# Optimization experiments

Hardware: AMD Instinct MI355X
Metric: run time of the kernel (lower is better)

The kernel has to match this reference:

```python
import jax, jax.numpy as jnp
import numpy as np

QMIN, QMAX = 0, 255        # 8-bit asymmetric activation quant bounds
GROUP_SIZE = 128

def setup_inputs() -> dict:
    key = jax.random.key(0)
    k1, k2, k3, k4, k5 = jax.random.split(key, 5)
    x = jax.random.normal(k1, (1, 2048, 4096), dtype=jnp.float32)
    qweight = jax.random.randint(k2, (4096, 32, 128), 0, 16, dtype=jnp.int32)  # uint4 codes
    w_scales = jax.random.uniform(k3, (4096, 32), dtype=jnp.float32, minval=0.001, maxval=0.02)
    w_zero_points = jax.random.randint(k4, (4096, 32), 0, 16, dtype=jnp.int32)
    bias = jax.random.normal(k5, (4096,), dtype=jnp.float32)
    return {"x": x, "qweight": qweight, "w_scales": w_scales,
            "w_zero_points": w_zero_points, "bias": bias}

def reference(x, qweight, w_scales, w_zero_points, bias):
    xf = x.astype(jnp.float32)
    # per-token (last-dim) asymmetric dynamic activation quantization
    xmin = jnp.min(xf, axis=-1, keepdims=True)
    xmax = jnp.max(xf, axis=-1, keepdims=True)
    x_scale = jnp.clip((xmax - xmin) / (QMAX - QMIN), 1e-5, None)
    x_zp = jnp.clip(jnp.round(-xmin / x_scale), QMIN, QMAX)
    q = jnp.clip(jnp.round(xf / x_scale) + x_zp, QMIN, QMAX)
    centered_x = (q - x_zp).reshape(*x.shape[:-1], -1, GROUP_SIZE)  # [B,S,G,C]
    # grouped weight dequant (zero-point centered)
    centered_w = qweight.astype(jnp.float32) - w_zero_points.astype(jnp.float32)[..., None]  # [O,G,C]
    acc = jnp.einsum('bsgc,ogc->bsog', centered_x, centered_w)  # [B,S,O,G]
    out = (acc * w_scales[None, None]).sum(axis=-1)  # apply per-group weight scales
    out = out * x_scale  # per-token activation scale
    out = out + bias
    return out
```

## Files before the change

kernel.cpp:

```cpp
#include <hip/hip_runtime.h>
#include <stdint.h>

#define M_DIM 2048
#define N_DIM 4096
#define K_DIM 4096
#define NGROUP 32
#define GSIZE 128

#define RQ_UP   (127.0f / 15.0f)
#define RQ_DOWN (15.0f / 127.0f)

#define BM 128
#define BN 128
#define KSLICE 64
#define NSLICE (K_DIM / KSLICE)
#define ASLOT (BM * KSLICE)
#define BSLOT (BN * KSLICE)

typedef __attribute__((ext_vector_type(4))) int int32x4_t;

static __device__ __forceinline__ void gl2lds16(const void* g, void* l) {
    auto gp = (const __attribute__((address_space(1))) unsigned int*)(uintptr_t)g;
    auto lp = (__attribute__((address_space(3))) unsigned int*)(uintptr_t)l;
    __builtin_amdgcn_global_load_lds(gp, lp, 16, 0, 0);
}

#define WAITVM_(N) asm volatile("s_waitcnt vmcnt(" #N ")" ::: "memory")
#define WAITVM(N) WAITVM_(N)
#define WAITLGKM_(N) asm volatile("s_waitcnt lgkmcnt(" #N ")" ::: "memory")
#define WAITLGKM(N) WAITLGKM_(N)
#define BARRIER() asm volatile("s_barrier" ::: "memory")

#define QUANT_BLOCKS M_DIM
#define DEQ_BLOCKS ((N_DIM * K_DIM) / 8 / 256)

__global__ __launch_bounds__(256) void prep_kernel(
        const float* __restrict__ x,
        const int* __restrict__ qw,
        const float* __restrict__ wsc,
        const int* __restrict__ wzp,
        char* __restrict__ A8,
        char* __restrict__ Bt8,
        float* __restrict__ xscale,
        float* __restrict__ xzpc,
        int* __restrict__ Sw)
{
    const int t = threadIdx.x;
    if (blockIdx.x < QUANT_BLOCKS) {
        const int s = blockIdx.x;
        const float* xrow = x + (size_t)s * K_DIM;

        float xv[16];
        float vmin = 1e38f, vmax = -1e38f;
#pragma unroll
        for (int p = 0; p < 4; ++p) {
            float4 v = *((const float4*)(xrow + p * 1024) + t);
            xv[p*4+0] = v.x; xv[p*4+1] = v.y; xv[p*4+2] = v.z; xv[p*4+3] = v.w;
            vmin = fminf(vmin, fminf(fminf(v.x, v.y), fminf(v.z, v.w)));
            vmax = fmaxf(vmax, fmaxf(fmaxf(v.x, v.y), fmaxf(v.z, v.w)));
        }
#pragma unroll
        for (int off = 32; off > 0; off >>= 1) {
            vmin = fminf(vmin, __shfl_xor(vmin, off));
            vmax = fmaxf(vmax, __shfl_xor(vmax, off));
        }
        __shared__ float smin[4], smax[4];
        const int wave = t >> 6;
        if ((t & 63) == 0) { smin[wave] = vmin; smax[wave] = vmax; }
        __syncthreads();
        vmin = fminf(fminf(smin[0], smin[1]), fminf(smin[2], smin[3]));
        vmax = fmaxf(fmaxf(smax[0], smax[1]), fmaxf(smax[2], smax[3]));

        float sc = (vmax - vmin) / 255.0f;
        sc = fmaxf(sc, 1e-5f);
        float zp = rintf(-vmin / sc);
        zp = fminf(fmaxf(zp, 0.0f), 255.0f);

#pragma unroll
        for (int p = 0; p < 4; ++p) {
            int b[4];
#pragma unroll
            for (int e = 0; e < 4; ++e) {
                float q = fminf(fmaxf(rintf(xv[p*4+e] / sc) + zp, 0.0f), 255.0f);
                b[e] = (int)q - 128;
            }
            unsigned pack = (b[0] & 0xff) | ((b[1] & 0xff) << 8) |
                            ((b[2] & 0xff) << 16) | ((b[3] & 0xff) << 24);
            *(unsigned*)(A8 + (size_t)s * K_DIM + p * 1024 + t * 4) = pack;
        }
        if (t == 0) { xscale[s] = sc; xzpc[s] = 128.0f - zp; }
    } else {
        const size_t base = ((size_t)(blockIdx.x - QUANT_BLOCKS) * 256 + t) * 8;
        const int n = (int)(base >> 12);
        const int g = (int)((base >> 7) & 31);
        const int zp = wzp[n * NGROUP + g];

        const int cl = t & 15;
        float2 wp = *(const float2*)(wsc + (size_t)n * NGROUP + cl * 2);
        float smx = fmaxf(wp.x, wp.y);
#pragma unroll
        for (int off = 1; off < 16; off <<= 1)
            smx = fmaxf(smx, __shfl_xor(smx, off));
        const float factor = wsc[n * NGROUP + g] * (RQ_UP / smx);

        int4 c0 = *(const int4*)(qw + base);
        int4 c1 = *(const int4*)(qw + base + 4);
        int w[8];
        w[0] = (int)rintf((float)(c0.x - zp) * factor);
        w[1] = (int)rintf((float)(c0.y - zp) * factor);
        w[2] = (int)rintf((float)(c0.z - zp) * factor);
        w[3] = (int)rintf((float)(c0.w - zp) * factor);
        w[4] = (int)rintf((float)(c1.x - zp) * factor);
        w[5] = (int)rintf((float)(c1.y - zp) * factor);
        w[6] = (int)rintf((float)(c1.z - zp) * factor);
        w[7] = (int)rintf((float)(c1.w - zp) * factor);
        uint2 pk;
        pk.x = (w[0] & 0xff) | ((w[1] & 0xff) << 8) | ((w[2] & 0xff) << 16) | ((w[3] & 0xff) << 24);
        pk.y = (w[4] & 0xff) | ((w[5] & 0xff) << 8) | ((w[6] & 0xff) << 16) | ((w[7] & 0xff) << 24);
        *(uint2*)(Bt8 + base) = pk;

        int s8 = w[0] + w[1] + w[2] + w[3] + w[4] + w[5] + w[6] + w[7];
#pragma unroll
        for (int off = 1; off < 16; off <<= 1) s8 += __shfl_xor(s8, off);
        if ((t & 15) == 0)
            Sw[n * NGROUP + g] = s8;
    }
}

__global__ __launch_bounds__(256, 2) void gemm_kernel(
        const char* __restrict__ A8,
        const char* __restrict__ Bt8,
        const float* __restrict__ xscale,
        const float* __restrict__ xzpc,
        const float* __restrict__ wsc,
        const int* __restrict__ Sw,
        const float* __restrict__ bias,
        float* __restrict__ out)
{
    __shared__ __align__(16) char As[4][ASLOT];
    __shared__ __align__(16) char Bs[4][BSLOT];
    __shared__ float fws_s[BN], wsf_s[BN];

    const int tid  = threadIdx.x;
    const int bn   = blockIdx.x;
    const int bm   = blockIdx.y;
    const int wave = tid >> 6;
    const int lane = tid & 63;
    const int wr   = wave >> 1;
    const int wcl  = wave & 1;
    const int lrow  = lane & 15;
    const int lquad = lane >> 4;

    if (tid < BN) {
        const int n = bn * BN + tid;
        const int4* s4 = (const int4*)(Sw + (size_t)n * NGROUP);
        int acc = 0;
#pragma unroll
        for (int p = 0; p < 8; ++p) { int4 v = s4[p]; acc += v.x + v.y + v.z + v.w; }
        const float4* w4 = (const float4*)(wsc + (size_t)n * NGROUP);
        float s = 0.f;
#pragma unroll
        for (int p = 0; p < 8; ++p) {
            float4 w = w4[p];
            s = fmaxf(s, fmaxf(fmaxf(w.x, w.y), fmaxf(w.z, w.w)));
        }
        const float fw = s * RQ_DOWN;
        fws_s[tid] = fw;
        wsf_s[tid] = fw * (float)acc;
    }
    asm volatile("s_waitcnt vmcnt(0) lgkmcnt(0)" ::: "memory");

    const char* Ab = A8  + (size_t)(bm * BM) * K_DIM;
    const char* Bb = Bt8 + (size_t)(bn * BN) * K_DIM;
    const int lsub = lane >> 2;
    const int csrc = (lane & 3) ^ ((lane >> 3) & 3);
    const char* gA0 = Ab + (size_t)((wave * 16     ) + lsub) * K_DIM + csrc * 16;
    const char* gA1 = Ab + (size_t)((wave * 16 + 64) + lsub) * K_DIM + csrc * 16;
    const char* gB0 = Bb + (size_t)((wave * 16     ) + lsub) * K_DIM + csrc * 16;
    const char* gB1 = Bb + (size_t)((wave * 16 + 64) + lsub) * K_DIM + csrc * 16;
    const int lOF = wave * 1024;

    const int xq = (lquad ^ ((lrow >> 1) & 3)) * 16;
    int aoff[4], boff[4];
#pragma unroll
    for (int i = 0; i < 4; ++i)
        aoff[i] = (wr * 64 + i * 16 + lrow) * KSLICE + xq;
#pragma unroll
    for (int j = 0; j < 4; ++j)
        boff[j] = (wcl * 64 + j * 16 + lrow) * KSLICE + xq;

    int32x4_t iacc[4][4];
    const int32x4_t zi = {0, 0, 0, 0};
#pragma unroll
    for (int i = 0; i < 4; ++i)
#pragma unroll
        for (int j = 0; j < 4; ++j) iacc[i][j] = zi;

    int32x4_t aX[4], bX[4], aY[4], bY[4];

#define STAGE(t) {                                                    \
        const int sl_ = (t) & 3;                                      \
        const size_t k0_ = (size_t)(t) * KSLICE;                      \
        gl2lds16(gA0 + k0_, &As[sl_][0] + lOF);                       \
        gl2lds16(gA1 + k0_, &As[sl_][0] + 4096 + lOF);                \
        gl2lds16(gB0 + k0_, &Bs[sl_][0] + lOF);                       \
        gl2lds16(gB1 + k0_, &Bs[sl_][0] + 4096 + lOF);                \
    }

#define READF(t, af, bf) {                                            \
        const char* Ap_ = &As[(t) & 3][0];                            \
        const char* Bp_ = &Bs[(t) & 3][0];                            \
        _Pragma("unroll")                                             \
        for (int i_ = 0; i_ < 4; ++i_)                                \
            af[i_] = *(const int32x4_t*)(Ap_ + aoff[i_]);             \
        _Pragma("unroll")                                             \
        for (int j_ = 0; j_ < 4; ++j_)                                \
            bf[j_] = *(const int32x4_t*)(Bp_ + boff[j_]);             \
    }

#define MFMAS(af, bf) {                                               \
        __builtin_amdgcn_s_setprio(1);                                \
        _Pragma("unroll")                                             \
        for (int i_ = 0; i_ < 4; ++i_)                                \
            _Pragma("unroll")                                         \
            for (int j_ = 0; j_ < 4; ++j_)                            \
                iacc[i_][j_] = __builtin_amdgcn_mfma_i32_16x16x64_i8( \
                    af[i_], bf[j_], iacc[i_][j_], 0, 0, 0);           \
        __builtin_amdgcn_s_setprio(0);                                \
    }

#define BODY(s, VMN, CA, CB, NA, NB) {                                \
        if ((s) + 3 < NSLICE) STAGE((s) + 3);                         \
        WAITVM(VMN);                                                  \
        BARRIER();                                                    \
        READF((s) + 1, NA, NB);                                       \
        WAITLGKM(8);                                                  \
        __builtin_amdgcn_sched_barrier(0);                            \
        MFMAS(CA, CB);                                                \
        BARRIER();                                                    \
    }

    STAGE(0); STAGE(1); STAGE(2);
    WAITVM(8);
    BARRIER();
    READF(0, aX, bX);

    for (int s = 0; s < NSLICE - 4; s += 2) {
        BODY(s,     8, aX, bX, aY, bY);
        BODY(s + 1, 8, aY, bY, aX, bX);
    }
    BODY(60, 8, aX, bX, aY, bY);
    BODY(61, 4, aY, bY, aX, bX);
    WAITVM(0);
    BARRIER();
    READF(63, aY, bY);
    WAITLGKM(8);
    __builtin_amdgcn_sched_barrier(0);
    MFMAS(aX, bX);
    WAITLGKM(0);
    __builtin_amdgcn_sched_barrier(0);
    MFMAS(aY, bY);

    float fn[4], wf[4], bb[4];
    int ncol[4];
#pragma unroll
    for (int j = 0; j < 4; ++j) {
        const int ncl = wcl * 64 + j * 16 + lrow;
        ncol[j] = bn * BN + ncl;
        fn[j] = fws_s[ncl];
        wf[j] = wsf_s[ncl];
        bb[j] = bias[ncol[j]];
    }
    const int m0 = bm * BM + wr * 64;
#pragma unroll
    for (int i = 0; i < 4; ++i) {
#pragma unroll
        for (int r = 0; r < 4; ++r) {
            const int m = m0 + i * 16 + lquad * 4 + r;
            const float xs  = xscale[m];
            const float czp = xzpc[m];
            float* orow = out + (size_t)m * N_DIM;
#pragma unroll
            for (int j = 0; j < 4; ++j)
                orow[ncol[j]] = xs * (fn[j] * (float)iacc[i][j][r] + czp * wf[j]) + bb[j];
        }
    }
#undef BODY
#undef MFMAS
#undef READF
#undef STAGE
}

extern "C" void kernel_launch(void* const* d_in, const int* in_sizes, int n_in,
                              void* d_out, int out_size, void* d_ws, size_t ws_size,
                              hipStream_t stream) {
    const float* x     = (const float*)d_in[0];
    const int*   qw    = (const int*)d_in[1];
    const float* wsc   = (const float*)d_in[2];
    const int*   wzp   = (const int*)d_in[3];
    const float* bias  = (const float*)d_in[4];
    float* out = (float*)d_out;

    char* A8  = (char*)d_ws;
    char* Bt8 = A8 + (size_t)M_DIM * K_DIM;
    float* xscale = (float*)(Bt8 + (size_t)N_DIM * K_DIM);
    float* xzpc   = xscale + M_DIM;
    int*   Sw     = (int*)(xzpc + M_DIM);

    prep_kernel<<<QUANT_BLOCKS + DEQ_BLOCKS, 256, 0, stream>>>(
        x, qw, wsc, wzp, A8, Bt8, xscale, xzpc, Sw);
    dim3 grid(N_DIM / BN, M_DIM / BM);
    gemm_kernel<<<grid, 256, 0, stream>>>(A8, Bt8, xscale, xzpc, wsc, Sw, bias, out);
}
```

Before: 172.1 us.

## Replace register double-buffered LDS reads with inline-asm reads and single-buffer main loop

Removes the register ping-pong of A/B fragments. Each slice's eight ds_read_b128 are now issued in inline asm with a full lgkmcnt(0) wait, followed immediately by that slice's MFMAs, with the vmcnt wait adjusted to 12 for the deeper prefetch. Wait macros are wrapped in scheduling barriers, and the activation quantization uses a reciprocal multiply instead of division. This cuts VGPR pressure and simplifies scheduling, but LDS read latency is no longer overlapped with the previous slice's MFMAs, and the reciprocal can change rounding at boundaries.

```diff
diff --git a/kernel.cpp b/kernel.cpp
--- a/kernel.cpp
+++ b/kernel.cpp
@@ -25,11 +25,13 @@
     __builtin_amdgcn_global_load_lds(gp, lp, 16, 0, 0);
 }
 
-#define WAITVM_(N) asm volatile("s_waitcnt vmcnt(" #N ")" ::: "memory")
-#define WAITVM(N) WAITVM_(N)
-#define WAITLGKM_(N) asm volatile("s_waitcnt lgkmcnt(" #N ")" ::: "memory")
-#define WAITLGKM(N) WAITLGKM_(N)
-#define BARRIER() asm volatile("s_barrier" ::: "memory")
+#define WAITVM_(N) asm volatile("s_waitcnt vmcnt(" #N ")")
+#define WAITVM(N)                                   \
+    do {                                            \
+        __builtin_amdgcn_sched_barrier(0);          \
+        WAITVM_(N);                                 \
+        __builtin_amdgcn_sched_barrier(0);          \
+    } while (0)
 
 #define QUANT_BLOCKS M_DIM
 #define DEQ_BLOCKS ((N_DIM * K_DIM) / 8 / 256)
@@ -75,13 +77,14 @@
         sc = fmaxf(sc, 1e-5f);
         float zp = rintf(-vmin / sc);
         zp = fminf(fmaxf(zp, 0.0f), 255.0f);
+        const float inv_sc = 1.0f / sc;
 
 #pragma unroll
         for (int p = 0; p < 4; ++p) {
             int b[4];
 #pragma unroll
             for (int e = 0; e < 4; ++e) {
-                float q = fminf(fmaxf(rintf(xv[p*4+e] / sc) + zp, 0.0f), 255.0f);
+                float q = fminf(fmaxf(rintf(xv[p*4+e] * inv_sc) + zp, 0.0f), 255.0f);
                 b[e] = (int)q - 128;
             }
             unsigned pack = (b[0] & 0xff) | ((b[1] & 0xff) << 8) |
@@ -168,7 +171,9 @@
         fws_s[tid] = fw;
         wsf_s[tid] = fw * (float)acc;
     }
-    asm volatile("s_waitcnt vmcnt(0) lgkmcnt(0)" ::: "memory");
+    __builtin_amdgcn_sched_barrier(0);
+    asm volatile("s_waitcnt vmcnt(0) lgkmcnt(0)");
+    __builtin_amdgcn_sched_barrier(0);
 
     const char* Ab = A8  + (size_t)(bm * BM) * K_DIM;
     const char* Bb = Bt8 + (size_t)(bn * BN) * K_DIM;
@@ -181,13 +186,10 @@
     const int lOF = wave * 1024;
 
     const int xq = (lquad ^ ((lrow >> 1) & 3)) * 16;
-    int aoff[4], boff[4];
-#pragma unroll
-    for (int i = 0; i < 4; ++i)
-        aoff[i] = (wr * 64 + i * 16 + lrow) * KSLICE + xq;
-#pragma unroll
-    for (int j = 0; j < 4; ++j)
-        boff[j] = (wcl * 64 + j * 16 + lrow) * KSLICE + xq;
+    const unsigned asBase = (unsigned)(uintptr_t)&As[0][0];
+    const unsigned bsBase = (unsigned)(uintptr_t)&Bs[0][0];
+    const unsigned aOff0 = (unsigned)((wr  * 64 + lrow) * KSLICE + xq);
+    const unsigned bOff0 = (unsigned)((wcl * 64 + lrow) * KSLICE + xq);
 
     int32x4_t iacc[4][4];
     const int32x4_t zi = {0, 0, 0, 0};
@@ -195,8 +197,6 @@
     for (int i = 0; i < 4; ++i)
 #pragma unroll
         for (int j = 0; j < 4; ++j) iacc[i][j] = zi;
-
-    int32x4_t aX[4], bX[4], aY[4], bY[4];
 
 #define STAGE(t) {                                                    \
         const int sl_ = (t) & 3;                                      \
@@ -207,59 +207,53 @@
         gl2lds16(gB1 + k0_, &Bs[sl_][0] + 4096 + lOF);                \
     }
 
-#define READF(t, af, bf) {                                            \
-        const char* Ap_ = &As[(t) & 3][0];                            \
-        const char* Bp_ = &Bs[(t) & 3][0];                            \
-        _Pragma("unroll")                                             \
-        for (int i_ = 0; i_ < 4; ++i_)                                \
-            af[i_] = *(const int32x4_t*)(Ap_ + aoff[i_]);             \
-        _Pragma("unroll")                                             \
-        for (int j_ = 0; j_ < 4; ++j_)                                \
-            bf[j_] = *(const int32x4_t*)(Bp_ + boff[j_]);             \
-    }
-
-#define MFMAS(af, bf) {                                               \
+#define READ8(aAdr, bAdr, a0, a1, a2, a3, b0, b1, b2, b3)             \
+    asm volatile(                                                     \
+        "ds_read_b128 %0, %8 offset:0\n\t"                            \
+        "ds_read_b128 %1, %8 offset:1024\n\t"                         \
+        "ds_read_b128 %2, %8 offset:2048\n\t"                         \
+        "ds_read_b128 %3, %8 offset:3072\n\t"                         \
+        "ds_read_b128 %4, %9 offset:0\n\t"                            \
+        "ds_read_b128 %5, %9 offset:1024\n\t"                         \
+        "ds_read_b128 %6, %9 offset:2048\n\t"                         \
+        "ds_read_b128 %7, %9 offset:3072\n\t"                         \
+        "s_waitcnt lgkmcnt(0)"                                        \
+        : "=&v"(a0), "=&v"(a1), "=&v"(a2), "=&v"(a3),                 \
+          "=&v"(b0), "=&v"(b1), "=&v"(b2), "=&v"(b3)                  \
+        : "v"(aAdr), "v"(bAdr))
+
+#define MFMAS(a0, a1, a2, a3, b0, b1, b2, b3) {                       \
+        int32x4_t av_[4] = {a0, a1, a2, a3};                          \
+        int32x4_t bv_[4] = {b0, b1, b2, b3};                          \
         __builtin_amdgcn_s_setprio(1);                                \
         _Pragma("unroll")                                             \
         for (int i_ = 0; i_ < 4; ++i_)                                \
             _Pragma("unroll")                                         \
             for (int j_ = 0; j_ < 4; ++j_)                            \
                 iacc[i_][j_] = __builtin_amdgcn_mfma_i32_16x16x64_i8( \
-                    af[i_], bf[j_], iacc[i_][j_], 0, 0, 0);           \
+                    av_[i_], bv_[j_], iacc[i_][j_], 0, 0, 0);         \
         __builtin_amdgcn_s_setprio(0);                                \
     }
 
-#define BODY(s, VMN, CA, CB, NA, NB) {                                \
-        if ((s) + 3 < NSLICE) STAGE((s) + 3);                         \
+#define BODY(s, VMN, DOSTAGE) {                                       \
+        if (DOSTAGE) STAGE((s) + 3);                                  \
         WAITVM(VMN);                                                  \
-        BARRIER();                                                    \
-        READF((s) + 1, NA, NB);                                       \
-        WAITLGKM(8);                                                  \
-        __builtin_amdgcn_sched_barrier(0);                            \
-        MFMAS(CA, CB);                                                \
-        BARRIER();                                                    \
+        __builtin_amdgcn_s_barrier();                                 \
+        const unsigned sl_ = (unsigned)((s) & 3) * 8192u;             \
+        int32x4_t a0_, a1_, a2_, a3_, b0_, b1_, b2_, b3_;             \
+        READ8(asBase + sl_ + aOff0, bsBase + sl_ + bOff0,             \
+              a0_, a1_, a2_, a3_, b0_, b1_, b2_, b3_);                \
+        MFMAS(a0_, a1_, a2_, a3_, b0_, b1_, b2_, b3_);                \
+        __builtin_amdgcn_s_barrier();                                 \
     }
 
     STAGE(0); STAGE(1); STAGE(2);
-    WAITVM(8);
-    BARRIER();
-    READF(0, aX, bX);
-
-    for (int s = 0; s < NSLICE - 4; s += 2) {
-        BODY(s,     8, aX, bX, aY, bY);
-        BODY(s + 1, 8, aY, bY, aX, bX);
-    }
-    BODY(60, 8, aX, bX, aY, bY);
-    BODY(61, 4, aY, bY, aX, bX);
-    WAITVM(0);
-    BARRIER();
-    READF(63, aY, bY);
-    WAITLGKM(8);
-    __builtin_amdgcn_sched_barrier(0);
-    MFMAS(aX, bX);
-    WAITLGKM(0);
-    __builtin_amdgcn_sched_barrier(0);
-    MFMAS(aY, bY);
+
+    for (int s = 0; s <= NSLICE - 4; ++s)
+        BODY(s, 12, 1);
+    BODY(NSLICE - 3, 8, 0);
+    BODY(NSLICE - 2, 4, 0);
+    BODY(NSLICE - 1, 0, 0);
 
     float fn[4], wf[4], bb[4];
     int ncol[4];
@@ -287,7 +281,7 @@
     }
 #undef BODY
 #undef MFMAS
-#undef READF
+#undef READ8
 #undef STAGE
 }
 
```

Measured after the change: 176.2 us. 1.02x slower.
